# Optimization experiments

Measured on AMD Instinct MI355X. Metric: run time of the kernel, lower is better.

Reference implementation:

```python
import jax, jax.numpy as jnp
import numpy as np
from jax.scipy.stats import norm

K = 2               # select_experts
NOISE_EPS = 0.01
LOSS_COEF = 0.01
CV_EPS = 1e-10


def setup_inputs() -> dict:
    key = jax.random.key(0)
    ks = jax.random.split(key, 8)
    N, D, H, E = 8192, 1024, 4096, 8
    s_in = 1.0 / np.sqrt(D)
    s_h = 1.0 / np.sqrt(H)
    return {
        "x": jax.random.normal(ks[0], (N, D), jnp.float32),
        "noise": jax.random.normal(ks[1], (N, E), jnp.float32),
        "w_gate": jax.random.normal(ks[2], (D, E), jnp.float32) * s_in,
        "w_noise": jax.random.normal(ks[3], (D, E), jnp.float32) * s_in,
        "W1": jax.random.normal(ks[4], (E, D, H), jnp.float32) * s_in,
        "b1": jnp.zeros((E, H), jnp.float32),
        "W2": jax.random.normal(ks[5], (E, H, D), jnp.float32) * s_h,
        "b2": jnp.zeros((E, D), jnp.float32),
    }


def _cv_squared(v):
    # torch .var() is unbiased (ddof=1)
    return v.var(ddof=1) / (v.mean() ** 2 + CV_EPS)


def reference(x, noise, w_gate, w_noise, W1, b1, W2, b2):
    N = x.shape[0]
    # --- noisy top-k gating (training path) ---
    clean_logits = x @ w_gate                                  # [N, E]
    noise_stddev = jax.nn.softplus(x @ w_noise) + NOISE_EPS    # [N, E]
    noisy_logits = clean_logits + noise * noise_stddev         # [N, E]
    top_vals, top_idx = jax.lax.top_k(noisy_logits, K + 1)     # [N, K+1]
    top_k_gates = jax.nn.softmax(top_vals[:, :K], axis=1)      # [N, K]
    gates = jnp.zeros_like(noisy_logits).at[
        jnp.arange(N)[:, None], top_idx[:, :K]
    ].set(top_k_gates)                                         # [N, E]

    # --- load (prob of being in top-k under the gating noise) ---
    thr_in = top_vals[:, K:K + 1]                              # [N, 1]
    thr_out = top_vals[:, K - 1:K]                             # [N, 1]
    is_in = noisy_logits > thr_in
    prob_in = norm.cdf((clean_logits - thr_in) / noise_stddev)
    prob_out = norm.cdf((clean_logits - thr_out) / noise_stddev)
    load = jnp.where(is_in, prob_in, prob_out).sum(0)          # [E]

    importance = gates.sum(0)                                  # [E]
    loss = (_cv_squared(importance) + _cv_squared(load)) * LOSS_COEF

    # --- dense all-expert stack, masked by sparse gates ---
    h = jax.nn.relu(jnp.einsum('nd,edh->neh', x, W1) + b1)     # [N, E, H]
    out = jnp.einsum('neh,ehd->ned', h, W2) + b2               # [N, E, D]
    y = jnp.einsum('ned,ne->nd', out, gates)                   # [N, D]
    return y, loss
```

## Files before the change

### kernel.cpp

```cpp
#include <hip/hip_runtime.h>

typedef unsigned short u16;
typedef unsigned int u32;
typedef __attribute__((ext_vector_type(4))) float f32x4;
typedef __attribute__((ext_vector_type(8))) short short8;
typedef __attribute__((ext_vector_type(4))) unsigned short u16x4;

#define BARR __builtin_amdgcn_s_barrier()
#define VM4  asm volatile("s_waitcnt vmcnt(4)" ::: "memory")
#define VM0  asm volatile("s_waitcnt vmcnt(0)" ::: "memory")

__device__ __forceinline__ u16 f2b(float f){
  u32 u = __float_as_uint(f);
  u = (u + 0x7FFFu + ((u >> 16) & 1u)) >> 16;
  return (u16)u;
}
__device__ __forceinline__ float b2f(u16 h){ return __uint_as_float(((u32)h) << 16); }

__device__ __forceinline__ void gload16(const void* g, void* l){
  __builtin_amdgcn_global_load_lds((__attribute__((address_space(1))) void*)(g),
                                   (__attribute__((address_space(3))) void*)(l), 16, 0, 0);
}

__global__ __launch_bounds__(256) void transpose_cvt_kernel(const float* __restrict__ src,
                                                            u16* __restrict__ dst,
                                                            int R, int C){
  __shared__ float t[64][65];
  int e = blockIdx.z;
  size_t eo = (size_t)R * C * e;
  int c0 = blockIdx.x * 64, r0 = blockIdx.y * 64;
  int tid = threadIdx.x;
  int lr = tid >> 4, lc4 = (tid & 15) * 4;
  #pragma unroll
  for (int i = 0; i < 4; i++){
    int r = lr + i * 16;
    float4 v = *(const float4*)&src[eo + (size_t)(r0 + r) * C + c0 + lc4];
    t[r][lc4] = v.x; t[r][lc4 + 1] = v.y; t[r][lc4 + 2] = v.z; t[r][lc4 + 3] = v.w;
  }
  __syncthreads();
  #pragma unroll
  for (int i = 0; i < 4; i++){
    int c = lr + i * 16;
    u16x4 o = { f2b(t[lc4][c]), f2b(t[lc4 + 1][c]), f2b(t[lc4 + 2][c]), f2b(t[lc4 + 3][c]) };
    *(u16x4*)&dst[eo + (size_t)(c0 + c) * R + r0 + lc4] = o;
  }
}

__global__ __launch_bounds__(256) void gating_kernel(const float* __restrict__ x,
                                                     const float* __restrict__ nz,
                                                     const float* __restrict__ wg,
                                                     const float* __restrict__ wn,
                                                     int* __restrict__ counts,
                                                     int4* __restrict__ rowinfo,
                                                     float* __restrict__ loadrow,
                                                     u16* __restrict__ xb){
  __shared__ float wpart[16][4][17];
  int tid = threadIdx.x, w = tid >> 6, lane = tid & 63;
  int d0 = w * 256 + lane * 4;
  float4 wgA[4], wgB[4], wnA[4], wnB[4];
  #pragma unroll
  for (int k = 0; k < 4; k++){
    wgA[k] = *(const float4*)&wg[(d0 + k) * 8];
    wgB[k] = *(const float4*)&wg[(d0 + k) * 8 + 4];
    wnA[k] = *(const float4*)&wn[(d0 + k) * 8];
    wnB[k] = *(const float4*)&wn[(d0 + k) * 8 + 4];
  }
  int rbase = blockIdx.x * 16;
  for (int r = 0; r < 16; r++){
    int row = rbase + r;
    float4 xv = *(const float4*)&x[(size_t)row * 1024 + d0];
    u16x4 xo = { f2b(xv.x), f2b(xv.y), f2b(xv.z), f2b(xv.w) };
    *(u16x4*)&xb[(size_t)row * 1024 + d0] = xo;
    float ag[8], an[8];
    #pragma unroll
    for (int e = 0; e < 8; e++){ ag[e] = 0.f; an[e] = 0.f; }
    float xk[4] = { xv.x, xv.y, xv.z, xv.w };
    #pragma unroll
    for (int k = 0; k < 4; k++){
      ag[0] = fmaf(xk[k], wgA[k].x, ag[0]); ag[1] = fmaf(xk[k], wgA[k].y, ag[1]);
      ag[2] = fmaf(xk[k], wgA[k].z, ag[2]); ag[3] = fmaf(xk[k], wgA[k].w, ag[3]);
      ag[4] = fmaf(xk[k], wgB[k].x, ag[4]); ag[5] = fmaf(xk[k], wgB[k].y, ag[5]);
      ag[6] = fmaf(xk[k], wgB[k].z, ag[6]); ag[7] = fmaf(xk[k], wgB[k].w, ag[7]);
      an[0] = fmaf(xk[k], wnA[k].x, an[0]); an[1] = fmaf(xk[k], wnA[k].y, an[1]);
      an[2] = fmaf(xk[k], wnA[k].z, an[2]); an[3] = fmaf(xk[k], wnA[k].w, an[3]);
      an[4] = fmaf(xk[k], wnB[k].x, an[4]); an[5] = fmaf(xk[k], wnB[k].y, an[5]);
      an[6] = fmaf(xk[k], wnB[k].z, an[6]); an[7] = fmaf(xk[k], wnB[k].w, an[7]);
    }
    #pragma unroll
    for (int off = 32; off >= 1; off >>= 1){
      #pragma unroll
      for (int e = 0; e < 8; e++){
        ag[e] += __shfl_xor(ag[e], off, 64);
        an[e] += __shfl_xor(an[e], off, 64);
      }
    }
    if (lane == 0){
      #pragma unroll
      for (int e = 0; e < 8; e++){
        wpart[r][w][e] = ag[e];
        wpart[r][w][8 + e] = an[e];
      }
    }
  }
  __syncthreads();
  if (tid < 16){
    int r = tid, row = rbase + r;
    float cg[16];
    #pragma unroll
    for (int v = 0; v < 16; v++)
      cg[v] = wpart[r][0][v] + wpart[r][1][v] + wpart[r][2][v] + wpart[r][3][v];
    float clean[8], sd[8], noisy[8];
    #pragma unroll
    for (int e = 0; e < 8; e++){
      clean[e] = cg[e];
      float v = cg[8 + e];
      float sp = fmaxf(v, 0.f) + log1pf(expf(-fabsf(v)));
      sd[e] = sp + 0.01f;
      noisy[e] = clean[e] + nz[row * 8 + e] * sd[e];
    }
    int i0 = 0, i1 = -1;
    float b0 = -3.4e38f, b1v = -3.4e38f, b2v = -3.4e38f;
    #pragma unroll
    for (int j = 0; j < 8; j++){
      float t = noisy[j];
      if (t > b0){ b2v = b1v; b1v = b0; i1 = i0; b0 = t; i0 = j; }
      else if (t > b1v){ b2v = b1v; b1v = t; i1 = j; }
      else if (t > b2v){ b2v = t; }
    }
    float eg = expf(b1v - b0);
    float g0 = 1.f / (1.f + eg), g1 = eg / (1.f + eg);
    rowinfo[row] = make_int4(i0, i1, __float_as_int(g0), __float_as_int(g1));
    atomicAdd(&counts[i0], 1);
    atomicAdd(&counts[i1], 1);
    float thr_in = b2v, thr_out = b1v;
    #pragma unroll
    for (int e = 0; e < 8; e++){
      bool isin = noisy[e] > thr_in;
      float thr = isin ? thr_in : thr_out;
      float z = (clean[e] - thr) / sd[e];
      loadrow[row * 8 + e] = 0.5f * (1.f + erff(z * 0.70710678118654752f));
    }
  }
}

__global__ __launch_bounds__(256) void fill_kernel(const int* __restrict__ counts,
                                                   const int4* __restrict__ rowinfo,
                                                   int* __restrict__ offs,
                                                   int* __restrict__ cnt2,
                                                   int* __restrict__ tok,
                                                   int* __restrict__ slot_of,
                                                   int* __restrict__ btab){
  __shared__ int loff[8];
  if (threadIdx.x == 0){
    int s = 0;
    for (int e = 0; e < 8; e++){ loff[e] = s; s += counts[e]; }
    if (blockIdx.x == 0){
      int nb = 0;
      for (int e = 0; e < 8; e++){
        offs[e] = loff[e];
        int nbe = (counts[e] + 255) >> 8;
        for (int t = 0; t < nbe; t++) btab[nb++] = (e << 16) | t;
      }
      offs[15] = nb;
    }
  }
  __syncthreads();
  int r = blockIdx.x * 256 + threadIdx.x;
  int4 ri = rowinfo[r];
  int p0 = atomicAdd(&cnt2[ri.x], 1);
  int s0 = loff[ri.x] + p0;
  tok[s0] = r; slot_of[2 * r] = s0;
  int p1 = atomicAdd(&cnt2[ri.y], 1);
  int s1 = loff[ri.y] + p1;
  tok[s1] = r; slot_of[2 * r + 1] = s1;
}

template<int KDIM, bool GATHER, bool RELU, bool PSPLIT>
__global__ __launch_bounds__(512, 1) void ffn8_kernel(
    const u16* __restrict__ Ag, const u16* __restrict__ Bt,
    const float* __restrict__ bias, u16* __restrict__ outp,
    const int* __restrict__ counts, const int* __restrict__ offs,
    const int* __restrict__ btab, const int* __restrict__ tok,
    int nc, int klen, int ostr, size_t pstride)
{
  __shared__ u16 SMEM[65536];
  u16 (*As)[2][8192] = (u16(*)[2][8192])SMEM;
  u16 (*Bs)[2][8192] = (u16(*)[2][8192])(SMEM + 32768);

  int gx = gridDim.x;
  int lin = blockIdx.y * gx + blockIdx.x;
  int total = gx * gridDim.y, chunk = total >> 3;
  int swz = (lin & 7) * chunk + (lin >> 3);
  int bx = swz % gx, tq = swz / gx;
  int nblk = offs[15];
  if (bx >= nblk) return;
  int kh = tq / nc;
  int tn = tq - kh * nc;
  int kbase = kh * klen;
  int niter = klen >> 7;
  int et = btab[bx]; int e = et >> 16, tm = et & 0xffff;
  int cnt = counts[e], off_e = offs[e];

  int tid = threadIdx.x, lane = tid & 63;
  int wid = tid >> 6, wm = wid >> 2, wn = wid & 3;

  int rl0 = tid >> 3, c8 = tid & 7;
  const char* Abase = (const char*)Ag + (size_t)kbase * 2;
  const char* Bbase = (const char*)(Bt + (size_t)e * 4194304) + (size_t)kbase * 2;
  u32 aoff[4], boff[4];
  #pragma unroll
  for (int h = 0; h < 2; h++)
    #pragma unroll
    for (int r = 0; r < 2; r++){
      int rl = h * 128 + r * 64 + rl0;
      int c8s = c8 ^ (rl & 7);
      int rr = tm * 256 + rl;
      int rc = (rr < cnt) ? rr : (cnt - 1);
      size_t arow = GATHER ? (size_t)tok[off_e + rc] : (size_t)(off_e + rc);
      aoff[h * 2 + r] = (u32)(arow * (KDIM * 2) + c8s * 16);
      boff[h * 2 + r] = (u32)((size_t)(tn * 256 + rl) * (KDIM * 2) + c8s * 16);
    }
  int ldst = (tid & ~63) * 8;

  auto stA = [&](int b, int h, int t){
    const char* s = Abase + (size_t)t * 128;
    gload16(s + aoff[h * 2 + 0], &As[b][h][ldst]);
    gload16(s + aoff[h * 2 + 1], &As[b][h][4096 + ldst]);
  };
  auto stB = [&](int b, int h, int t){
    const char* s = Bbase + (size_t)t * 128;
    gload16(s + boff[h * 2 + 0], &Bs[b][h][ldst]);
    gload16(s + boff[h * 2 + 1], &Bs[b][h][4096 + ldst]);
  };

  int lm = lane & 15, lkb = (lane >> 4) * 8;
  short8 Ar[4][2], Br[2][2][2];
  auto ldA = [&](int b, int rh){
    #pragma unroll
    for (int ii = 0; ii < 4; ii++){
      int rl = rh * 64 + ii * 16 + lm;
      #pragma unroll
      for (int ks = 0; ks < 2; ks++){
        int idx = (rl * 64 + ks * 32 + lkb) ^ ((rl & 7) << 3);
        Ar[ii][ks] = *(const short8*)&As[b][wm][idx];
      }
    }
  };
  auto ldB = [&](int b, int ch){
    #pragma unroll
    for (int jj = 0; jj < 2; jj++){
      int rb = wn * 64 + ch * 32 + jj * 16 + lm;
      int hB = rb >> 7, rl = rb & 127;
      #pragma unroll
      for (int ks = 0; ks < 2; ks++){
        int idx = (rl * 64 + ks * 32 + lkb) ^ ((rl & 7) << 3);
        Br[ch][jj][ks] = *(const short8*)&Bs[b][hB][idx];
      }
    }
  };

  f32x4 acc[8][4];
  #pragma unroll
  for (int i = 0; i < 8; i++)
    #pragma unroll
    for (int j = 0; j < 4; j++) acc[i][j] = (f32x4){0.f, 0.f, 0.f, 0.f};

  auto mfmaQ = [&](int rh, int ch){
    __builtin_amdgcn_s_setprio(1);
    #pragma unroll
    for (int ks = 0; ks < 2; ks++)
      #pragma unroll
      for (int ii = 0; ii < 4; ii++)
        #pragma unroll
        for (int jj = 0; jj < 2; jj++)
          acc[rh * 4 + ii][ch * 2 + jj] = __builtin_amdgcn_mfma_f32_16x16x32_bf16(
              Ar[ii][ks], Br[ch][jj][ks], acc[rh * 4 + ii][ch * 2 + jj], 0, 0, 0);
    __builtin_amdgcn_s_setprio(0);
  };

  stA(0, 0, 0); stA(0, 1, 0); stB(0, 0, 0); stB(0, 1, 0);
  stB(1, 0, 1); stA(1, 0, 1);
  VM4; BARR;

  for (int j = 0; j < niter - 1; ++j){
    int t1 = 2 * j + 1, t2 = 2 * j + 2, t3 = 2 * j + 3;
    ldA(0, 0); ldB(0, 0);
    stA(1, 1, t1);
    BARR; mfmaQ(0, 0); ldB(0, 1); BARR;
    stB(1, 1, t1);
    BARR; mfmaQ(0, 1); ldA(0, 1); BARR;
    stB(0, 0, t2);
    BARR; mfmaQ(1, 1); BARR;
    stA(0, 0, t2);
    BARR; mfmaQ(1, 0); VM4; BARR;
    ldA(1, 0); ldB(1, 0);
    stA(0, 1, t2);
    BARR; mfmaQ(0, 0); ldB(1, 1); BARR;
    stB(0, 1, t2);
    BARR; mfmaQ(0, 1); ldA(1, 1); BARR;
    stB(1, 0, t3);
    BARR; mfmaQ(1, 1); BARR;
    stA(1, 0, t3);
    BARR; mfmaQ(1, 0); VM4; BARR;
  }

  {
    int t1 = (klen >> 6) - 1;
    ldA(0, 0); ldB(0, 0);
    stA(1, 1, t1);
    BARR; mfmaQ(0, 0); ldB(0, 1); BARR;
    stB(1, 1, t1);
    BARR; mfmaQ(0, 1); ldA(0, 1); BARR;
    BARR; mfmaQ(1, 1); BARR;
    mfmaQ(1, 0); VM0; BARR;
    ldA(1, 0); ldB(1, 0);
    BARR; mfmaQ(0, 0); ldB(1, 1); BARR;
    BARR; mfmaQ(0, 1); ldA(1, 1); BARR;
    BARR; mfmaQ(1, 1); BARR;
    mfmaQ(1, 0);
  }

  BARR;
  u16* po = outp + (PSPLIT ? (size_t)kh * pstride : 0);
  int lr4 = (lane >> 4) * 4;
  #pragma unroll
  for (int i = 0; i < 8; i++){
    int rl = wm * 128 + i * 16 + lr4;
    #pragma unroll
    for (int jj = 0; jj < 4; jj++){
      int col = wn * 64 + jj * 16 + lm;
      float bv = PSPLIT ? 0.f : bias[e * ostr + tn * 256 + col];
      #pragma unroll
      for (int q = 0; q < 4; q++){
        int row = rl + q;
        float v = acc[i][jj][q] + bv;
        if (RELU) v = fmaxf(v, 0.f);
        int g = (col >> 3) ^ (row & 7);
        SMEM[row * 256 + (g << 3) + (col & 7)] = f2b(v);
      }
    }
  }
  BARR;
  int srow = tid >> 5;
  int scg  = tid & 31;
  #pragma unroll
  for (int p = 0; p < 16; p++){
    int row = p * 16 + srow;
    int g = scg ^ (row & 7);
    short8 vv = *(const short8*)&SMEM[row * 256 + (g << 3)];
    int grow = tm * 256 + row;
    if (grow < cnt){
      *(short8*)(po + (size_t)(off_e + grow) * ostr + tn * 256 + (scg << 3)) = vv;
    }
  }
}

__global__ __launch_bounds__(256) void combine_kernel(const u16* __restrict__ pb,
                                                      const float* __restrict__ b2,
                                                      const int4* __restrict__ rowinfo,
                                                      const int* __restrict__ slot_of,
                                                      float* __restrict__ y){
  const size_t PS = (size_t)16384 * 1024;
  int w = threadIdx.x >> 6, lane = threadIdx.x & 63;
  int row = blockIdx.x * 4 + w;
  int4 ri = rowinfo[row];
  float g0 = __int_as_float(ri.z), g1 = __int_as_float(ri.w);
  int s0 = slot_of[2 * row], s1 = slot_of[2 * row + 1];
  const u16* pa = pb + ((size_t)s0 << 10);
  const u16* pbb = pb + ((size_t)s1 << 10);
  #pragma unroll
  for (int k = 0; k < 4; k++){
    int c4 = k * 256 + lane * 4;
    float4 sum0 = *(const float4*)&b2[(ri.x << 10) + c4];
    float4 sum1 = *(const float4*)&b2[(ri.y << 10) + c4];
    #pragma unroll
    for (int kh = 0; kh < 4; kh++){
      u16x4 a = *(const u16x4*)&pa[kh * PS + c4];
      u16x4 b = *(const u16x4*)&pbb[kh * PS + c4];
      sum0.x += b2f(a.x); sum0.y += b2f(a.y); sum0.z += b2f(a.z); sum0.w += b2f(a.w);
      sum1.x += b2f(b.x); sum1.y += b2f(b.y); sum1.z += b2f(b.z); sum1.w += b2f(b.w);
    }
    float4 o;
    o.x = g0 * sum0.x + g1 * sum1.x;
    o.y = g0 * sum0.y + g1 * sum1.y;
    o.z = g0 * sum0.z + g1 * sum1.z;
    o.w = g0 * sum0.w + g1 * sum1.w;
    *(float4*)&y[(size_t)row * 1024 + c4] = o;
  }
}

__global__ __launch_bounds__(256) void loss1_kernel(const int4* __restrict__ rowinfo,
                                                    const float* __restrict__ loadrow,
                                                    float* __restrict__ partials){
  __shared__ float part[16][256];
  int tid = threadIdx.x;
  int r = blockIdx.x * 256 + tid;
  int4 ri = rowinfo[r];
  float g0 = __int_as_float(ri.z), g1 = __int_as_float(ri.w);
  f32x4 l0 = *(const f32x4*)&loadrow[r * 8];
  f32x4 l1 = *(const f32x4*)&loadrow[r * 8 + 4];
  #pragma unroll
  for (int e = 0; e < 8; e++){
    part[e][tid] = ((ri.x == e) ? g0 : 0.f) + ((ri.y == e) ? g1 : 0.f);
    part[8 + e][tid] = (e < 4) ? l0[e & 3] : l1[e & 3];
  }
  __syncthreads();
  #pragma unroll
  for (int s = 128; s >= 1; s >>= 1){
    if (tid < s){
      #pragma unroll
      for (int e = 0; e < 16; e++) part[e][tid] += part[e][tid + s];
    }
    __syncthreads();
  }
  if (tid < 16) partials[blockIdx.x * 16 + tid] = part[tid][0];
}

__global__ __launch_bounds__(64) void loss2_kernel(const float* __restrict__ partials,
                                                   float* __restrict__ out_loss){
  __shared__ float tot[16];
  int tid = threadIdx.x;
  if (tid < 16){
    float s = 0.f;
    for (int b = 0; b < 32; b++) s += partials[b * 16 + tid];
    tot[tid] = s;
  }
  __syncthreads();
  if (tid == 0){
    float mi = 0.f, ml = 0.f;
    for (int e = 0; e < 8; e++){ mi += tot[e]; ml += tot[8 + e]; }
    mi *= 0.125f; ml *= 0.125f;
    float vi = 0.f, vl = 0.f;
    for (int e = 0; e < 8; e++){
      float di = tot[e] - mi; vi += di * di;
      float dl = tot[8 + e] - ml; vl += dl * dl;
    }
    vi /= 7.f; vl /= 7.f;
    float cvi = vi / (mi * mi + 1e-10f);
    float cvl = vl / (ml * ml + 1e-10f);
    out_loss[0] = 0.01f * (cvi + cvl);
  }
}

extern "C" void kernel_launch(void* const* d_in, const int* in_sizes, int n_in,
                              void* d_out, int out_size, void* d_ws, size_t ws_size,
                              hipStream_t stream){
  const float* x  = (const float*)d_in[0];
  const float* nz = (const float*)d_in[1];
  const float* wg = (const float*)d_in[2];
  const float* wn = (const float*)d_in[3];
  const float* W1 = (const float*)d_in[4];
  const float* b1 = (const float*)d_in[5];
  const float* W2 = (const float*)d_in[6];
  const float* b2 = (const float*)d_in[7];
  float* y = (float*)d_out;
  float* loss = y + (size_t)8192 * 1024;

  char* ws = (char*)d_ws;
  size_t o = 0;
  auto alloc = [&](size_t bytes){ size_t r = o; o += (bytes + 255) & ~(size_t)255; return r; };
  int*  counts  = (int*)(ws + alloc(64));
  int*  cnt2    = (int*)(ws + alloc(64));
  int*  offs    = (int*)(ws + alloc(64));
  int*  btab    = (int*)(ws + alloc(1024));
  int4* rowinfo = (int4*)(ws + alloc((size_t)8192 * 16));
  int*  slot_of = (int*)(ws + alloc((size_t)16384 * 4));
  int*  tok     = (int*)(ws + alloc((size_t)16384 * 4));
  float* loadrow = (float*)(ws + alloc((size_t)8192 * 8 * 4));
  float* partials = (float*)(ws + alloc(32 * 16 * 4));
  u16*  xb      = (u16*)(ws + alloc((size_t)8192 * 1024 * 2));
  u16*  w1t     = (u16*)(ws + alloc((size_t)8 * 1024 * 4096 * 2));
  u16*  w2t     = (u16*)(ws + alloc((size_t)8 * 1024 * 4096 * 2));
  u16*  h_buf   = (u16*)(ws + alloc((size_t)16384 * 4096 * 2));
  u16*  pbuf    = (u16*)(ws + alloc((size_t)4 * 16384 * 1024 * 2));
  if (o > ws_size) return;

  hipMemsetAsync(ws, 0, 768, stream);

  gating_kernel<<<512, 256, 0, stream>>>(x, nz, wg, wn, counts, rowinfo, loadrow, xb);
  transpose_cvt_kernel<<<dim3(64, 16, 8), 256, 0, stream>>>(W1, w1t, 1024, 4096);
  transpose_cvt_kernel<<<dim3(16, 64, 8), 256, 0, stream>>>(W2, w2t, 4096, 1024);
  fill_kernel<<<32, 256, 0, stream>>>(counts, rowinfo, offs, cnt2, tok, slot_of, btab);
  ffn8_kernel<1024, true, true, false><<<dim3(72, 16), 512, 0, stream>>>(
      xb, w1t, b1, h_buf, counts, offs, btab, tok, 16, 1024, 4096, 0);
  ffn8_kernel<4096, false, false, true><<<dim3(72, 16), 512, 0, stream>>>(
      h_buf, w2t, nullptr, pbuf, counts, offs, btab, tok, 4, 1024, 1024,
      (size_t)16384 * 1024);
  combine_kernel<<<2048, 256, 0, stream>>>(pbuf, b2, rowinfo, slot_of, y);
  loss1_kernel<<<32, 256, 0, stream>>>(rowinfo, loadrow, partials);
  loss2_kernel<<<1, 64, 0, stream>>>(partials, loss);
}
```

Measured before the change: 710.0 us.

## Merge weight transpose launches and drop LDS-staged epilogue in expert GEMM

Fuses the two weight transpose/convert launches into one grid that picks W1 or W2 from the z index, saving a kernel launch. The GEMM epilogue no longer stages bf16 results through swizzled shared memory for coalesced 16-byte stores. Each lane now writes scalar 2-byte values straight to global memory. This removes two barriers and the LDS round trip, but the global stores become narrow and poorly coalesced.

```diff
diff --git a/kernel.cpp b/kernel.cpp
--- a/kernel.cpp
+++ b/kernel.cpp
@@ -22,13 +22,22 @@
                                    (__attribute__((address_space(3))) void*)(l), 16, 0, 0);
 }
 
-__global__ __launch_bounds__(256) void transpose_cvt_kernel(const float* __restrict__ src,
-                                                            u16* __restrict__ dst,
-                                                            int R, int C){
+__global__ __launch_bounds__(256) void transpose_cvt2_kernel(const float* __restrict__ W1,
+                                                             const float* __restrict__ W2,
+                                                             u16* __restrict__ w1t,
+                                                             u16* __restrict__ w2t){
   __shared__ float t[64][65];
-  int e = blockIdx.z;
-  size_t eo = (size_t)R * C * e;
-  int c0 = blockIdx.x * 64, r0 = blockIdx.y * 64;
+  int z = blockIdx.z;
+  const float* src; u16* dst; int R, C, c0, r0; size_t eo;
+  if (z < 8){
+    src = W1; dst = w1t; R = 1024; C = 4096;
+    c0 = blockIdx.x * 64; r0 = blockIdx.y * 64;
+    eo = (size_t)R * C * z;
+  } else {
+    src = W2; dst = w2t; R = 4096; C = 1024;
+    c0 = blockIdx.y * 64; r0 = blockIdx.x * 64;
+    eo = (size_t)R * C * (z - 8);
+  }
   int tid = threadIdx.x;
   int lr = tid >> 4, lc4 = (tid & 15) * 4;
   #pragma unroll
@@ -183,9 +192,8 @@
     const int* __restrict__ btab, const int* __restrict__ tok,
     int nc, int klen, int ostr, size_t pstride)
 {
-  __shared__ u16 SMEM[65536];
-  u16 (*As)[2][8192] = (u16(*)[2][8192])SMEM;
-  u16 (*Bs)[2][8192] = (u16(*)[2][8192])(SMEM + 32768);
+  __shared__ u16 As[2][2][128 * 64];
+  __shared__ u16 Bs[2][2][128 * 64];
 
   int gx = gridDim.x;
   int lin = blockIdx.y * gx + blockIdx.x;
@@ -320,37 +328,24 @@
     mfmaQ(1, 0);
   }
 
-  BARR;
+  int lr = (lane >> 4) * 4;
   u16* po = outp + (PSPLIT ? (size_t)kh * pstride : 0);
-  int lr4 = (lane >> 4) * 4;
   #pragma unroll
   for (int i = 0; i < 8; i++){
-    int rl = wm * 128 + i * 16 + lr4;
+    int row_l = wm * 128 + i * 16 + lr;
     #pragma unroll
     for (int jj = 0; jj < 4; jj++){
-      int col = wn * 64 + jj * 16 + lm;
-      float bv = PSPLIT ? 0.f : bias[e * ostr + tn * 256 + col];
+      int col = tn * 256 + wn * 64 + jj * 16 + lm;
+      float bv = PSPLIT ? 0.f : bias[e * ostr + col];
       #pragma unroll
       for (int q = 0; q < 4; q++){
-        int row = rl + q;
-        float v = acc[i][jj][q] + bv;
-        if (RELU) v = fmaxf(v, 0.f);
-        int g = (col >> 3) ^ (row & 7);
-        SMEM[row * 256 + (g << 3) + (col & 7)] = f2b(v);
-      }
-    }
-  }
-  BARR;
-  int srow = tid >> 5;
-  int scg  = tid & 31;
-  #pragma unroll
-  for (int p = 0; p < 16; p++){
-    int row = p * 16 + srow;
-    int g = scg ^ (row & 7);
-    short8 vv = *(const short8*)&SMEM[row * 256 + (g << 3)];
-    int grow = tm * 256 + row;
-    if (grow < cnt){
-      *(short8*)(po + (size_t)(off_e + grow) * ostr + tn * 256 + (scg << 3)) = vv;
+        int r = tm * 256 + row_l + q;
+        if (r < cnt){
+          float v = acc[i][jj][q] + bv;
+          if (RELU) v = fmaxf(v, 0.f);
+          po[(size_t)(off_e + r) * ostr + col] = f2b(v);
+        }
+      }
     }
   }
 }
@@ -478,8 +473,7 @@
   hipMemsetAsync(ws, 0, 768, stream);
 
   gating_kernel<<<512, 256, 0, stream>>>(x, nz, wg, wn, counts, rowinfo, loadrow, xb);
-  transpose_cvt_kernel<<<dim3(64, 16, 8), 256, 0, stream>>>(W1, w1t, 1024, 4096);
-  transpose_cvt_kernel<<<dim3(16, 64, 8), 256, 0, stream>>>(W2, w2t, 4096, 1024);
+  transpose_cvt2_kernel<<<dim3(64, 16, 16), 256, 0, stream>>>(W1, W2, w1t, w2t);
   fill_kernel<<<32, 256, 0, stream>>>(counts, rowinfo, offs, cnt2, tok, slot_of, btab);
   ffn8_kernel<1024, true, true, false><<<dim3(72, 16), 512, 0, stream>>>(
       xb, w1t, b1, h_buf, counts, offs, btab, tok, 16, 1024, 4096, 0);
```

Result: faster. 683.6 us (-3.7%).
